# Kernel optimization log

Measured on AMD Instinct MI355X. Metric: run time of the kernel, lower is better.

Reference implementation:

```python
import jax, jax.numpy as jnp
import numpy as np

NUM_GRID = 16
GRID_SIZE = 8  # 128 / NUM_GRID
H = W = 128
BN_EPS = 1e-5


def conv2d(x, w, b, pad):
    y = jax.lax.conv_general_dilated(
        x, w, window_strides=(1, 1), padding=[(pad, pad), (pad, pad)],
        dimension_numbers=('NCHW', 'OIHW', 'NCHW'))
    return y + b[None, :, None, None]


def bn(x, g, be, m, v):
    # inference-mode BatchNorm2d with running stats
    inv = g / jnp.sqrt(v + BN_EPS)
    return x * inv[None, :, None, None] + (be - m * inv)[None, :, None, None]


def setup_inputs() -> dict:
    key = jax.random.key(0)
    ks = jax.random.split(key, 6)
    def wconv(k, o, i, s):
        return jax.random.normal(k, (o, i, s, s), jnp.float32) * (1.0 / np.sqrt(i * s * s))
    return {
        'x': jax.random.uniform(ks[0], (64, 1, 128, 128), jnp.float32),
        'w1': wconv(ks[1], 64, 1, 3), 'b1': jnp.zeros((64,), jnp.float32),
        'g1': jnp.ones((64,), jnp.float32), 'be1': jnp.zeros((64,), jnp.float32),
        'm1': jnp.zeros((64,), jnp.float32), 'v1': jnp.ones((64,), jnp.float32),
        'w2': wconv(ks[2], 32, 64, 3), 'b2': jnp.zeros((32,), jnp.float32),
        'g2': jnp.ones((32,), jnp.float32), 'be2': jnp.zeros((32,), jnp.float32),
        'm2': jnp.zeros((32,), jnp.float32), 'v2': jnp.ones((32,), jnp.float32),
        'w3': wconv(ks[3], 32, 32, 3), 'b3': jnp.zeros((32,), jnp.float32),
        'g3': jnp.ones((32,), jnp.float32), 'be3': jnp.zeros((32,), jnp.float32),
        'm3': jnp.zeros((32,), jnp.float32), 'v3': jnp.ones((32,), jnp.float32),
        'w4': wconv(ks[4], 1, 32, 3), 'b4': jnp.zeros((1,), jnp.float32),
    }


def reference(x, w1, b1, g1, be1, m1, v1, w2, b2, g2, be2, m2, v2,
              w3, b3, g3, be3, m3, v3, w4, b4):
    # EncoderAttentionNodes.forward, phase='train', expressed with static shapes:
    # instead of torch.nonzero gather of valid grids, compute per-grid node
    # coordinates for ALL 16x16 grids and return a validity mask. The math per
    # valid grid is identical (the rect mask is a rectangular 8x8 block, so
    # masking + normalization reduce to block-local weighted sums).
    B = x.shape[0]
    h = jax.nn.relu(bn(conv2d(x, w1, b1, 4), g1, be1, m1, v1))   # [B,64,134,134]
    h = jax.nn.relu(bn(conv2d(h, w2, b2, 0), g2, be2, m2, v2))   # [B,32,132,132]
    h = jax.nn.relu(bn(conv2d(h, w3, b3, 0), g3, be3, m3, v3))   # [B,32,130,130]
    heat_raw = conv2d(h, w4, b4, 0)                              # [B,1,128,128]
    heat = jax.nn.sigmoid(heat_raw)[:, 0]                        # [B,128,128]

    # block view: [B, yi, ya, xj, xc] with yi,xj grid indices and ya,xc in-block
    hb = heat.reshape(B, NUM_GRID, GRID_SIZE, NUM_GRID, GRID_SIZE)
    grid = hb.max(axis=(2, 4)).reshape(B, NUM_GRID * NUM_GRID)   # maxpool 8x8 s8
    sorted_grid = jnp.sort(grid, axis=1)[:, ::-1]                # descending
    thresh = jnp.maximum(sorted_grid[:, 16], 0.9)[:, None]       # train phase
    valid = grid > thresh                                        # [B,256]

    xref = jnp.linspace(0.0, 1.0, W).reshape(NUM_GRID, GRID_SIZE)
    yref = jnp.linspace(0.0, 1.0, H).reshape(NUM_GRID, GRID_SIZE)
    s = hb.sum(axis=(2, 4))                                      # [B,16,16] block mass
    sx = jnp.einsum('biajc,jc->bij', hb, xref)
    sy = jnp.einsum('biajc,ia->bij', hb, yref)
    nodes = jnp.stack([sx / s, sy / s], axis=-1)                 # [B,16,16,2]
    nodes = nodes.reshape(B, NUM_GRID * NUM_GRID, 2)
    nodes = jnp.where(valid[:, :, None], nodes, 0.0)             # zero padded slots
    nodes_per_image = valid.sum(axis=1).astype(jnp.int32)        # == torch.bincount
    return nodes, heat_raw, valid, nodes_per_image
```

## Files before the change

kernel.cpp:

```cpp
#include <hip/hip_runtime.h>
#include <math.h>

#define BN_EPS 1e-5f

typedef _Float16 half8 __attribute__((ext_vector_type(8)));
typedef float f32x4 __attribute__((ext_vector_type(4)));

__global__ __launch_bounds__(256) void prep_kernel(
    const float* __restrict__ w1, const float* __restrict__ b1,
    const float* __restrict__ g1, const float* __restrict__ be1,
    const float* __restrict__ m1, const float* __restrict__ v1,
    const float* __restrict__ w2, const float* __restrict__ b2,
    const float* __restrict__ g2, const float* __restrict__ be2,
    const float* __restrict__ m2, const float* __restrict__ v2,
    const float* __restrict__ w3, const float* __restrict__ b3,
    const float* __restrict__ g3, const float* __restrict__ be3,
    const float* __restrict__ m3, const float* __restrict__ v3,
    char* __restrict__ ws)
{
    float* w1e = (float*)ws;
    float* b1e = (float*)(ws + 2304);
    float* b2e = (float*)(ws + 2560);
    float* b3e = (float*)(ws + 2688);
    _Float16* wT2e = (_Float16*)(ws + 2816);
    _Float16* wT3e = (_Float16*)(ws + 39680);

    for (int t = threadIdx.x; t < 576; t += 256) {
        int oc = t / 9;
        float inv = g1[oc] * rsqrtf(v1[oc] + BN_EPS);
        w1e[t] = w1[t] * inv;
    }
    for (int t = threadIdx.x; t < 64; t += 256) {
        float inv = g1[t] * rsqrtf(v1[t] + BN_EPS);
        b1e[t] = b1[t] * inv + be1[t] - m1[t] * inv;
    }
    for (int t = threadIdx.x; t < 32; t += 256) {
        float inv2 = g2[t] * rsqrtf(v2[t] + BN_EPS);
        b2e[t] = b2[t] * inv2 + be2[t] - m2[t] * inv2;
        float inv3 = g3[t] * rsqrtf(v3[t] + BN_EPS);
        b3e[t] = b3[t] * inv3 + be3[t] - m3[t] * inv3;
    }
    for (int t = threadIdx.x; t < 18432; t += 256) {
        int r = t / 2048; int rem = t - r * 2048;
        int oc = rem >> 6; int ic = rem & 63;
        float inv = g2[oc] * rsqrtf(v2[oc] + BN_EPS);
        wT2e[t] = (_Float16)(w2[(oc * 64 + ic) * 9 + r] * inv);
    }
    for (int t = threadIdx.x; t < 9216; t += 256) {
        int r = t / 1024; int rem = t - r * 1024;
        int oc = rem >> 5; int ic = rem & 31;
        float inv = g3[oc] * rsqrtf(v3[oc] + BN_EPS);
        wT3e[t] = (_Float16)(w3[(oc * 32 + ic) * 9 + r] * inv);
    }
}

__global__ __launch_bounds__(256, 3) void f12_kernel(
    const float* __restrict__ x, const char* __restrict__ wsw,
    _Float16* __restrict__ h2)
{
    const float* w1e = (const float*)wsw;
    const float* b1e = (const float*)(wsw + 2304);
    const float* b2e = (const float*)(wsw + 2560);
    const _Float16* wT2e = (const _Float16*)(wsw + 2816);

    constexpr int PSTR = 36;
    __shared__ float sX[20 * 20];
    __shared__ _Float16 sH1[324 * PSTR];

    const int t = threadIdx.x, lane = t & 63, w = t >> 6;
    const int tl = lane & 15, g = lane >> 4;
    const int img = blockIdx.z;
    const int x0 = blockIdx.x * 16, y0 = blockIdx.y * 16;

    const float* xb = x + (size_t)img * 16384;
    for (int idx = t; idx < 400; idx += 256) {
        int r = idx / 20, c = idx - r * 20;
        int iy = y0 - 4 + r, ix = x0 - 4 + c;
        sX[idx] = (iy >= 0 && iy < 128 && ix >= 0 && ix < 128)
                      ? xb[iy * 128 + ix] : 0.f;
    }
    __syncthreads();

    f32x4 acc[4][2];
#pragma unroll
    for (int pf = 0; pf < 4; pf++)
#pragma unroll
        for (int of = 0; of < 2; of++) acc[pf][of] = (f32x4){0.f, 0.f, 0.f, 0.f};

#pragma unroll
    for (int h = 0; h < 2; h++) {
        {
            const int ocg = __builtin_amdgcn_readfirstlane(t >> 6);
            const int pxslot = t & 63;
            float wreg[8][9];
            float bb[8];
#pragma unroll
            for (int j = 0; j < 8; j++) {
                int oc = h * 32 + ocg * 8 + j;
                bb[j] = b1e[oc];
#pragma unroll
                for (int k = 0; k < 9; k++) wreg[j][k] = w1e[oc * 9 + k];
            }
#pragma unroll
            for (int round = 0; round < 6; round++) {
                int px = pxslot + round * 64;
                if (px < 324) {
                    int py = px / 18, pxx = px - py * 18;
                    float a[9];
#pragma unroll
                    for (int ky = 0; ky < 3; ky++)
#pragma unroll
                        for (int kx = 0; kx < 3; kx++)
                            a[ky * 3 + kx] = sX[(py + ky) * 20 + pxx + kx];
                    half8 hv;
#pragma unroll
                    for (int j = 0; j < 8; j++) {
                        float acc1 = bb[j];
#pragma unroll
                        for (int k = 0; k < 9; k++)
                            acc1 = fmaf(a[k], wreg[j][k], acc1);
                        hv[j] = (_Float16)fmaxf(acc1, 0.f);
                    }
                    *(half8*)(&sH1[px * PSTR + ocg * 8]) = hv;
                }
            }
        }
        __syncthreads();

#pragma unroll
        for (int r = 0; r < 9; r++) {
            const int ky = r / 3, kx = r - ky * 3;
            half8 wf0 = *(const half8*)(
                wT2e + (r * 32 + tl) * 64 + h * 32 + g * 8);
            half8 wf1 = *(const half8*)(
                wT2e + (r * 32 + 16 + tl) * 64 + h * 32 + g * 8);
#pragma unroll
            for (int pf = 0; pf < 4; pf++) {
                const int yl = w * 4 + pf + ky;
                half8 af = *(const half8*)(
                    &sH1[(yl * 18 + tl + kx) * PSTR + g * 8]);
                acc[pf][0] = __builtin_amdgcn_mfma_f32_16x16x32_f16(
                    af, wf0, acc[pf][0], 0, 0, 0);
                acc[pf][1] = __builtin_amdgcn_mfma_f32_16x16x32_f16(
                    af, wf1, acc[pf][1], 0, 0, 0);
            }
        }
        if (h == 0) __syncthreads();
    }

    const float bb0 = b2e[tl], bb1 = b2e[16 + tl];
    _Float16* outb = h2 + (size_t)img * 132 * 132 * 32;
#pragma unroll
    for (int pf = 0; pf < 4; pf++) {
        int y = y0 + w * 4 + pf;
        if (y >= 132) continue;
#pragma unroll
        for (int i = 0; i < 4; i++) {
            int xc = x0 + 4 * g + i;
            if (xc >= 132) continue;
            _Float16* q = outb + ((size_t)y * 132 + xc) * 32 + tl;
            q[0]  = (_Float16)fmaxf(acc[pf][0][i] + bb0, 0.f);
            q[16] = (_Float16)fmaxf(acc[pf][1][i] + bb1, 0.f);
        }
    }
}

__global__ __launch_bounds__(256, 3) void conv3_kernel(
    const _Float16* __restrict__ in, const char* __restrict__ wsw,
    _Float16* __restrict__ out)
{
    const float* b3e = (const float*)(wsw + 2688);
    const _Float16* wT3e = (const _Float16*)(wsw + 39680);

    constexpr int HIN = 132, WIN = 132, HOUT = 130, WOUT = 130;
    constexpr int PSTR = 40;
    __shared__ _Float16 sIn[324 * PSTR];

    const int t = threadIdx.x, lane = t & 63, w = t >> 6;
    const int tl = lane & 15, g = lane >> 4;
    const int img = 63 - blockIdx.z;
    const int x0 = blockIdx.x * 16, y0 = blockIdx.y * 16;

    const _Float16* inb = in + (size_t)img * HIN * WIN * 32;

    for (int kk = 0; kk < 6; kk++) {
        int idx = t + kk * 256;
        if (idx < 1296) {
            int px = idx >> 2, sg = idx & 3;
            int py = px / 18, pxx = px - py * 18;
            int iy = y0 + py, ix = x0 + pxx;
            half8 v = (half8){0, 0, 0, 0, 0, 0, 0, 0};
            if (iy < HIN && ix < WIN)
                v = *(const half8*)(inb + ((size_t)iy * WIN + ix) * 32 + sg * 8);
            *(half8*)(&sIn[px * PSTR + sg * 8]) = v;
        }
    }

    f32x4 acc[4][2];
#pragma unroll
    for (int pf = 0; pf < 4; pf++)
#pragma unroll
        for (int of = 0; of < 2; of++) acc[pf][of] = (f32x4){0.f, 0.f, 0.f, 0.f};

    __syncthreads();

#pragma unroll
    for (int r = 0; r < 9; r++) {
        const int ky = r / 3, kx = r - ky * 3;
        half8 wf0 = *(const half8*)(wT3e + (r * 32 + tl) * 32 + g * 8);
        half8 wf1 = *(const half8*)(wT3e + (r * 32 + 16 + tl) * 32 + g * 8);
#pragma unroll
        for (int pf = 0; pf < 4; pf++) {
            const int yl = w * 4 + pf + ky;
            half8 af = *(const half8*)(&sIn[(yl * 18 + tl + kx) * PSTR + g * 8]);
            acc[pf][0] = __builtin_amdgcn_mfma_f32_16x16x32_f16(
                af, wf0, acc[pf][0], 0, 0, 0);
            acc[pf][1] = __builtin_amdgcn_mfma_f32_16x16x32_f16(
                af, wf1, acc[pf][1], 0, 0, 0);
        }
    }

    const float bb0 = b3e[tl], bb1 = b3e[16 + tl];
    _Float16* outb = out + (size_t)img * HOUT * WOUT * 32;
#pragma unroll
    for (int pf = 0; pf < 4; pf++) {
        int y = y0 + w * 4 + pf;
        if (y >= HOUT) continue;
#pragma unroll
        for (int i = 0; i < 4; i++) {
            int xc = x0 + 4 * g + i;
            if (xc >= WOUT) continue;
            _Float16* q = outb + ((size_t)y * WOUT + xc) * 32 + tl;
            q[0]  = (_Float16)fmaxf(acc[pf][0][i] + bb0, 0.f);
            q[16] = (_Float16)fmaxf(acc[pf][1][i] + bb1, 0.f);
        }
    }
}

__global__ __launch_bounds__(256) void conv4_kernel(
    const _Float16* __restrict__ h3, const float* __restrict__ w4,
    const float* __restrict__ b4, float* __restrict__ heat,
    float* __restrict__ stats)
{
    const int img = blockIdx.z;
    const int x0 = blockIdx.x * 16, y0 = blockIdx.y * 16;
    const int t = threadIdx.x;
    const int ty = t >> 4, tx = t & 15;

    __shared__ float sw[288];
    __shared__ float sS[256];
    for (int i = t; i < 288; i += 256) sw[i] = w4[i];
    __syncthreads();

    const int y = y0 + ty, x = x0 + tx;
    const _Float16* hb = h3 + (size_t)img * 130 * 130 * 32;
    float acc = b4[0];
#pragma unroll
    for (int r = 0; r < 9; r++) {
        const int ky = r / 3, kx = r - ky * 3;
        const _Float16* p = hb + ((size_t)(y + ky) * 130 + (x + kx)) * 32;
        half8 v0 = *(const half8*)(p);
        half8 v1 = *(const half8*)(p + 8);
        half8 v2 = *(const half8*)(p + 16);
        half8 v3 = *(const half8*)(p + 24);
#pragma unroll
        for (int j = 0; j < 8; j++) {
            acc = fmaf((float)v0[j], sw[(j) * 9 + r], acc);
            acc = fmaf((float)v1[j], sw[(8 + j) * 9 + r], acc);
            acc = fmaf((float)v2[j], sw[(16 + j) * 9 + r], acc);
            acc = fmaf((float)v3[j], sw[(24 + j) * 9 + r], acc);
        }
    }
    heat[(size_t)img * 16384 + y * 128 + x] = acc;
    sS[t] = 1.0f / (1.0f + expf(-acc));
    __syncthreads();

    const int w = t >> 6, l = t & 63;
    const int cy = w >> 1, cx = w & 1;
    const int ly = cy * 8 + (l >> 3), lx = cx * 8 + (l & 7);
    float v = sS[ly * 16 + lx];
    float mx = v, s = v;
    float sx = v * ((float)(x0 + lx) * (1.0f / 127.0f));
    float sy = v * ((float)(y0 + ly) * (1.0f / 127.0f));
#pragma unroll
    for (int off = 1; off < 64; off <<= 1) {
        mx = fmaxf(mx, __shfl_xor(mx, off));
        s += __shfl_xor(s, off);
        sx += __shfl_xor(sx, off);
        sy += __shfl_xor(sy, off);
    }
    if (l == 0) {
        int cell = (blockIdx.y * 2 + cy) * 16 + blockIdx.x * 2 + cx;
        float4* st = (float4*)(stats + ((size_t)img * 256 + cell) * 4);
        *st = make_float4(mx, s, sx, sy);
    }
}

__global__ __launch_bounds__(256) void nodes2_kernel(
    const float* __restrict__ stats, float* __restrict__ nodes,
    float* __restrict__ valid, float* __restrict__ counts)
{
    int b = blockIdx.x;
    int gsl = threadIdx.x;
    float4 st = ((const float4*)stats)[b * 256 + gsl];
    float mx = st.x, s = st.y, sx = st.z, sy = st.w;

    __shared__ float gv[256];
    gv[gsl] = mx;
    __syncthreads();

    int cgt = 0, ceq = 0;
    for (int j = 0; j < 256; j++) {
        float vj = gv[j];
        cgt += (vj > mx) ? 1 : 0;
        ceq += (vj == mx) ? 1 : 0;
    }
    __shared__ float kth;
    if (cgt <= 16 && 16 < cgt + ceq) kth = mx;
    __syncthreads();

    float thresh = fmaxf(kth, 0.9f);
    bool val = mx > thresh;
    nodes[((size_t)b * 256 + gsl) * 2 + 0] = val ? sx / s : 0.f;
    nodes[((size_t)b * 256 + gsl) * 2 + 1] = val ? sy / s : 0.f;
    valid[(size_t)b * 256 + gsl] = val ? 1.f : 0.f;

    unsigned long long ball = __ballot(val);
    __shared__ int wc[4];
    if ((gsl & 63) == 0) wc[gsl >> 6] = __popcll(ball);
    __syncthreads();
    if (gsl == 0) counts[b] = (float)(wc[0] + wc[1] + wc[2] + wc[3]);
}

extern "C" void kernel_launch(void* const* d_in, const int* in_sizes, int n_in,
                              void* d_out, int out_size, void* d_ws, size_t ws_size,
                              hipStream_t stream)
{
    const float* x   = (const float*)d_in[0];
    const float* w1  = (const float*)d_in[1];
    const float* b1  = (const float*)d_in[2];
    const float* g1  = (const float*)d_in[3];
    const float* be1 = (const float*)d_in[4];
    const float* m1  = (const float*)d_in[5];
    const float* v1  = (const float*)d_in[6];
    const float* w2  = (const float*)d_in[7];
    const float* b2  = (const float*)d_in[8];
    const float* g2  = (const float*)d_in[9];
    const float* be2 = (const float*)d_in[10];
    const float* m2  = (const float*)d_in[11];
    const float* v2  = (const float*)d_in[12];
    const float* w3  = (const float*)d_in[13];
    const float* b3  = (const float*)d_in[14];
    const float* g3  = (const float*)d_in[15];
    const float* be3 = (const float*)d_in[16];
    const float* m3  = (const float*)d_in[17];
    const float* v3  = (const float*)d_in[18];
    const float* w4  = (const float*)d_in[19];
    const float* b4  = (const float*)d_in[20];

    float* out = (float*)d_out;
    float* out_nodes = out;
    float* out_heat  = out + 32768;
    float* out_valid = out + 32768 + 1048576;
    float* out_count = out + 32768 + 1048576 + 16384;

    char* ws = (char*)d_ws;
    const size_t WREGION = 65536;
    float* stats = (float*)(ws + WREGION);
    _Float16* h2 = (_Float16*)(ws + WREGION + 262144);
    _Float16* h3 = h2 + (size_t)64 * 17424 * 32;

    prep_kernel<<<1, 256, 0, stream>>>(w1, b1, g1, be1, m1, v1,
                                       w2, b2, g2, be2, m2, v2,
                                       w3, b3, g3, be3, m3, v3, ws);

    dim3 gd(9, 9, 64);
    f12_kernel<<<gd, 256, 0, stream>>>(x, ws, h2);
    conv3_kernel<<<gd, 256, 0, stream>>>(h2, ws, h3);

    dim3 gd4(8, 8, 64);
    conv4_kernel<<<gd4, 256, 0, stream>>>(h3, w4, b4, out_heat, stats);

    nodes2_kernel<<<64, 256, 0, stream>>>(stats, out_nodes, out_valid, out_count);
}
```

Baseline: 241.3 us.

## Use fp16 dot2 for conv1 and overlap second conv1 half with conv2 MFMA

Conv1 weights are prepacked as fp16 pairs and the input tile is held in fp16 LDS, so each output channel needs five fdot2 instructions instead of nine fp32 FMAs. The second half of conv1 is computed into registers while the MFMA pass for the first half runs, and is written to shared memory only after a barrier. This hides scalar conv1 work behind matrix work. In exchange it holds more registers (occupancy hint drops from 3 to 2 blocks) and lowers conv1 input and weight precision to fp16.

```diff
diff --git a/kernel.cpp b/kernel.cpp
--- a/kernel.cpp
+++ b/kernel.cpp
@@ -4,7 +4,19 @@
 #define BN_EPS 1e-5f
 
 typedef _Float16 half8 __attribute__((ext_vector_type(8)));
+typedef _Float16 half2v __attribute__((ext_vector_type(2)));
 typedef float f32x4 __attribute__((ext_vector_type(4)));
+
+#if __has_builtin(__builtin_amdgcn_fdot2)
+#define FDOT2(a, b, c) __builtin_amdgcn_fdot2((a), (b), (c), false)
+#else
+#define FDOT2(a, b, c) \
+    fmaf((float)(a)[0], (float)(b)[0], fmaf((float)(a)[1], (float)(b)[1], (c)))
+#endif
+
+static __device__ inline half2v u2h(unsigned int u) {
+    union { unsigned int x; half2v h; } c; c.x = u; return c.h;
+}
 
 __global__ __launch_bounds__(256) void prep_kernel(
     const float* __restrict__ w1, const float* __restrict__ b1,
@@ -18,21 +30,27 @@
     const float* __restrict__ m3, const float* __restrict__ v3,
     char* __restrict__ ws)
 {
-    float* w1e = (float*)ws;
     float* b1e = (float*)(ws + 2304);
     float* b2e = (float*)(ws + 2560);
     float* b3e = (float*)(ws + 2688);
     _Float16* wT2e = (_Float16*)(ws + 2816);
     _Float16* wT3e = (_Float16*)(ws + 39680);
-
-    for (int t = threadIdx.x; t < 576; t += 256) {
-        int oc = t / 9;
-        float inv = g1[oc] * rsqrtf(v1[oc] + BN_EPS);
-        w1e[t] = w1[t] * inv;
-    }
+    unsigned int* w1p = (unsigned int*)(ws + 58112);
+
     for (int t = threadIdx.x; t < 64; t += 256) {
         float inv = g1[t] * rsqrtf(v1[t] + BN_EPS);
         b1e[t] = b1[t] * inv + be1[t] - m1[t] * inv;
+    }
+    for (int t = threadIdx.x; t < 320; t += 256) {
+        int oc = t / 5, p = t - oc * 5;
+        float inv = g1[oc] * rsqrtf(v1[oc] + BN_EPS);
+        int k0 = 2 * p, k1 = 2 * p + 1;
+        _Float16 h0 = (k0 < 9) ? (_Float16)(w1[oc * 9 + k0] * inv) : (_Float16)0.f;
+        _Float16 h1 = (k1 < 9) ? (_Float16)(w1[oc * 9 + k1] * inv) : (_Float16)0.f;
+        unsigned short u0, u1;
+        __builtin_memcpy(&u0, &h0, 2);
+        __builtin_memcpy(&u1, &h1, 2);
+        w1p[t] = (unsigned int)u0 | ((unsigned int)u1 << 16);
     }
     for (int t = threadIdx.x; t < 32; t += 256) {
         float inv2 = g2[t] * rsqrtf(v2[t] + BN_EPS);
@@ -54,17 +72,17 @@
     }
 }
 
-__global__ __launch_bounds__(256, 3) void f12_kernel(
+__global__ __launch_bounds__(256, 2) void f12_kernel(
     const float* __restrict__ x, const char* __restrict__ wsw,
     _Float16* __restrict__ h2)
 {
-    const float* w1e = (const float*)wsw;
     const float* b1e = (const float*)(wsw + 2304);
     const float* b2e = (const float*)(wsw + 2560);
     const _Float16* wT2e = (const _Float16*)(wsw + 2816);
+    const unsigned int* w1p = (const unsigned int*)(wsw + 58112);
 
     constexpr int PSTR = 36;
-    __shared__ float sX[20 * 20];
+    __shared__ _Float16 sXh[400];
     __shared__ _Float16 sH1[324 * PSTR];
 
     const int t = threadIdx.x, lane = t & 63, w = t >> 6;
@@ -76,10 +94,14 @@
     for (int idx = t; idx < 400; idx += 256) {
         int r = idx / 20, c = idx - r * 20;
         int iy = y0 - 4 + r, ix = x0 - 4 + c;
-        sX[idx] = (iy >= 0 && iy < 128 && ix >= 0 && ix < 128)
+        float v = (iy >= 0 && iy < 128 && ix >= 0 && ix < 128)
                       ? xb[iy * 128 + ix] : 0.f;
-    }
-    __syncthreads();
+        sXh[idx] = (_Float16)v;
+    }
+    __syncthreads();
+
+    const int ocg = __builtin_amdgcn_readfirstlane(t >> 6);
+    const int slot = t & 63;
 
     f32x4 acc[4][2];
 #pragma unroll
@@ -87,46 +109,59 @@
 #pragma unroll
         for (int of = 0; of < 2; of++) acc[pf][of] = (f32x4){0.f, 0.f, 0.f, 0.f};
 
-#pragma unroll
-    for (int h = 0; h < 2; h++) {
-        {
-            const int ocg = __builtin_amdgcn_readfirstlane(t >> 6);
-            const int pxslot = t & 63;
-            float wreg[8][9];
-            float bb[8];
+    half8 rr[6];
+
+    auto c1_compute = [&](int h) {
+        unsigned int wp[8][5];
+        float bb[8];
+#pragma unroll
+        for (int j = 0; j < 8; j++) {
+            int oc = h * 32 + ocg * 8 + j;
+            bb[j] = b1e[oc];
+#pragma unroll
+            for (int p = 0; p < 5; p++) wp[j][p] = w1p[oc * 5 + p];
+        }
+#pragma unroll
+        for (int round = 0; round < 6; round++) {
+            int px = slot + round * 64;
+            int pc = (px < 324) ? px : 0;
+            int py = pc / 18, pxx = pc - py * 18;
+            _Float16 tv[9];
+#pragma unroll
+            for (int r3 = 0; r3 < 3; r3++)
+#pragma unroll
+                for (int c3 = 0; c3 < 3; c3++)
+                    tv[r3 * 3 + c3] = sXh[(py + r3) * 20 + pxx + c3];
+            half2v a0 = {tv[0], tv[1]};
+            half2v a1 = {tv[2], tv[3]};
+            half2v a2 = {tv[4], tv[5]};
+            half2v a3 = {tv[6], tv[7]};
+            half2v a4 = {tv[8], (_Float16)0.f};
+            half8 q;
 #pragma unroll
             for (int j = 0; j < 8; j++) {
-                int oc = h * 32 + ocg * 8 + j;
-                bb[j] = b1e[oc];
-#pragma unroll
-                for (int k = 0; k < 9; k++) wreg[j][k] = w1e[oc * 9 + k];
+                float f = bb[j];
+                f = FDOT2(a0, u2h(wp[j][0]), f);
+                f = FDOT2(a1, u2h(wp[j][1]), f);
+                f = FDOT2(a2, u2h(wp[j][2]), f);
+                f = FDOT2(a3, u2h(wp[j][3]), f);
+                f = FDOT2(a4, u2h(wp[j][4]), f);
+                q[j] = (_Float16)fmaxf(f, 0.f);
             }
-#pragma unroll
-            for (int round = 0; round < 6; round++) {
-                int px = pxslot + round * 64;
-                if (px < 324) {
-                    int py = px / 18, pxx = px - py * 18;
-                    float a[9];
-#pragma unroll
-                    for (int ky = 0; ky < 3; ky++)
-#pragma unroll
-                        for (int kx = 0; kx < 3; kx++)
-                            a[ky * 3 + kx] = sX[(py + ky) * 20 + pxx + kx];
-                    half8 hv;
-#pragma unroll
-                    for (int j = 0; j < 8; j++) {
-                        float acc1 = bb[j];
-#pragma unroll
-                        for (int k = 0; k < 9; k++)
-                            acc1 = fmaf(a[k], wreg[j][k], acc1);
-                        hv[j] = (_Float16)fmaxf(acc1, 0.f);
-                    }
-                    *(half8*)(&sH1[px * PSTR + ocg * 8]) = hv;
-                }
-            }
-        }
-        __syncthreads();
-
+            rr[round] = q;
+        }
+    };
+
+    auto c1_store = [&]() {
+#pragma unroll
+        for (int round = 0; round < 6; round++) {
+            int px = slot + round * 64;
+            if (px < 324)
+                *(half8*)(&sH1[px * PSTR + ocg * 8]) = rr[round];
+        }
+    };
+
+    auto c2_mfma = [&](int h) {
 #pragma unroll
         for (int r = 0; r < 9; r++) {
             const int ky = r / 3, kx = r - ky * 3;
@@ -145,8 +180,19 @@
                     af, wf1, acc[pf][1], 0, 0, 0);
             }
         }
-        if (h == 0) __syncthreads();
-    }
+    };
+
+    c1_compute(0);
+    c1_store();
+    __syncthreads();
+
+    c1_compute(1);
+    c2_mfma(0);
+    __syncthreads();
+
+    c1_store();
+    __syncthreads();
+    c2_mfma(1);
 
     const float bb0 = b2e[tl], bb1 = b2e[16 + tl];
     _Float16* outb = h2 + (size_t)img * 132 * 132 * 32;
```

After: 260.5 us. 8.0% more time.

## Fuse conv3 and conv4 into one kernel, keeping h3 tile in shared memory

Applied to the files above, without the earlier changes.

Merges the conv3 and conv4 kernels so each block computes an 18x18 halo tile of conv3 output directly from global h2 and stores it in LDS, then runs conv4 and the per-cell statistics from LDS. This removes the global round trip for the h3 intermediate and one kernel launch. In exchange, halo pixels are recomputed (324 vs 256 per tile), conv3 inputs are read straight from global/cache rather than staged in LDS, and occupancy drops to 2 blocks per CU.

```diff
diff --git a/kernel.cpp b/kernel.cpp
--- a/kernel.cpp
+++ b/kernel.cpp
@@ -165,100 +165,67 @@
     }
 }
 
-__global__ __launch_bounds__(256, 3) void conv3_kernel(
-    const _Float16* __restrict__ in, const char* __restrict__ wsw,
-    _Float16* __restrict__ out)
+__global__ __launch_bounds__(256, 2) void f34_kernel(
+    const _Float16* __restrict__ h2, const char* __restrict__ wsw,
+    const float* __restrict__ w4, const float* __restrict__ b4,
+    float* __restrict__ heat, float* __restrict__ stats)
 {
     const float* b3e = (const float*)(wsw + 2688);
     const _Float16* wT3e = (const _Float16*)(wsw + 39680);
 
-    constexpr int HIN = 132, WIN = 132, HOUT = 130, WOUT = 130;
-    constexpr int PSTR = 40;
-    __shared__ _Float16 sIn[324 * PSTR];
+    constexpr int PSTR = 36;
+    __shared__ _Float16 sH3[324 * PSTR];
+    __shared__ float sw[288];
+    __shared__ float sS[256];
 
     const int t = threadIdx.x, lane = t & 63, w = t >> 6;
     const int tl = lane & 15, g = lane >> 4;
     const int img = 63 - blockIdx.z;
     const int x0 = blockIdx.x * 16, y0 = blockIdx.y * 16;
 
-    const _Float16* inb = in + (size_t)img * HIN * WIN * 32;
-
-    for (int kk = 0; kk < 6; kk++) {
-        int idx = t + kk * 256;
-        if (idx < 1296) {
-            int px = idx >> 2, sg = idx & 3;
-            int py = px / 18, pxx = px - py * 18;
-            int iy = y0 + py, ix = x0 + pxx;
-            half8 v = (half8){0, 0, 0, 0, 0, 0, 0, 0};
-            if (iy < HIN && ix < WIN)
-                v = *(const half8*)(inb + ((size_t)iy * WIN + ix) * 32 + sg * 8);
-            *(half8*)(&sIn[px * PSTR + sg * 8]) = v;
-        }
-    }
-
-    f32x4 acc[4][2];
-#pragma unroll
-    for (int pf = 0; pf < 4; pf++)
-#pragma unroll
-        for (int of = 0; of < 2; of++) acc[pf][of] = (f32x4){0.f, 0.f, 0.f, 0.f};
-
-    __syncthreads();
-
+    for (int i = t; i < 288; i += 256) sw[i] = w4[i];
+
+    const _Float16* inb = h2 + (size_t)img * 132 * 132 * 32;
+    const float bb0 = b3e[tl], bb1 = b3e[16 + tl];
+
+#pragma unroll
+    for (int tt = 0; tt < 6; tt++) {
+        const int m = w + 4 * tt;
+        if (m < 21) {
+            int px = m * 16 + tl;
+            if (px > 323) px = 323;
+            const int py = px / 18, pxx = px - py * 18;
+            const _Float16* base =
+                inb + ((size_t)(y0 + py) * 132 + (x0 + pxx)) * 32 + g * 8;
+            f32x4 c0 = (f32x4){0.f, 0.f, 0.f, 0.f};
+            f32x4 c1 = (f32x4){0.f, 0.f, 0.f, 0.f};
+#pragma unroll
+            for (int r = 0; r < 9; r++) {
+                const int ky = r / 3, kx = r - ky * 3;
+                half8 wf0 = *(const half8*)(wT3e + (r * 32 + tl) * 32 + g * 8);
+                half8 wf1 = *(const half8*)(wT3e + (r * 32 + 16 + tl) * 32 + g * 8);
+                half8 af = *(const half8*)(base + ((size_t)ky * 132 + kx) * 32);
+                c0 = __builtin_amdgcn_mfma_f32_16x16x32_f16(af, wf0, c0, 0, 0, 0);
+                c1 = __builtin_amdgcn_mfma_f32_16x16x32_f16(af, wf1, c1, 0, 0, 0);
+            }
+#pragma unroll
+            for (int i = 0; i < 4; i++) {
+                const int px_d = m * 16 + 4 * g + i;
+                if (px_d < 324) {
+                    sH3[px_d * PSTR + tl] = (_Float16)fmaxf(c0[i] + bb0, 0.f);
+                    sH3[px_d * PSTR + 16 + tl] = (_Float16)fmaxf(c1[i] + bb1, 0.f);
+                }
+            }
+        }
+    }
+    __syncthreads();
+
+    const int ty = t >> 4, tx = t & 15;
+    float acc = b4[0];
 #pragma unroll
     for (int r = 0; r < 9; r++) {
         const int ky = r / 3, kx = r - ky * 3;
-        half8 wf0 = *(const half8*)(wT3e + (r * 32 + tl) * 32 + g * 8);
-        half8 wf1 = *(const half8*)(wT3e + (r * 32 + 16 + tl) * 32 + g * 8);
-#pragma unroll
-        for (int pf = 0; pf < 4; pf++) {
-            const int yl = w * 4 + pf + ky;
-            half8 af = *(const half8*)(&sIn[(yl * 18 + tl + kx) * PSTR + g * 8]);
-            acc[pf][0] = __builtin_amdgcn_mfma_f32_16x16x32_f16(
-                af, wf0, acc[pf][0], 0, 0, 0);
-            acc[pf][1] = __builtin_amdgcn_mfma_f32_16x16x32_f16(
-                af, wf1, acc[pf][1], 0, 0, 0);
-        }
-    }
-
-    const float bb0 = b3e[tl], bb1 = b3e[16 + tl];
-    _Float16* outb = out + (size_t)img * HOUT * WOUT * 32;
-#pragma unroll
-    for (int pf = 0; pf < 4; pf++) {
-        int y = y0 + w * 4 + pf;
-        if (y >= HOUT) continue;
-#pragma unroll
-        for (int i = 0; i < 4; i++) {
-            int xc = x0 + 4 * g + i;
-            if (xc >= WOUT) continue;
-            _Float16* q = outb + ((size_t)y * WOUT + xc) * 32 + tl;
-            q[0]  = (_Float16)fmaxf(acc[pf][0][i] + bb0, 0.f);
-            q[16] = (_Float16)fmaxf(acc[pf][1][i] + bb1, 0.f);
-        }
-    }
-}
-
-__global__ __launch_bounds__(256) void conv4_kernel(
-    const _Float16* __restrict__ h3, const float* __restrict__ w4,
-    const float* __restrict__ b4, float* __restrict__ heat,
-    float* __restrict__ stats)
-{
-    const int img = blockIdx.z;
-    const int x0 = blockIdx.x * 16, y0 = blockIdx.y * 16;
-    const int t = threadIdx.x;
-    const int ty = t >> 4, tx = t & 15;
-
-    __shared__ float sw[288];
-    __shared__ float sS[256];
-    for (int i = t; i < 288; i += 256) sw[i] = w4[i];
-    __syncthreads();
-
-    const int y = y0 + ty, x = x0 + tx;
-    const _Float16* hb = h3 + (size_t)img * 130 * 130 * 32;
-    float acc = b4[0];
-#pragma unroll
-    for (int r = 0; r < 9; r++) {
-        const int ky = r / 3, kx = r - ky * 3;
-        const _Float16* p = hb + ((size_t)(y + ky) * 130 + (x + kx)) * 32;
+        const _Float16* p = &sH3[((ty + ky) * 18 + tx + kx) * PSTR];
         half8 v0 = *(const half8*)(p);
         half8 v1 = *(const half8*)(p + 8);
         half8 v2 = *(const half8*)(p + 16);
@@ -271,12 +238,12 @@
             acc = fmaf((float)v3[j], sw[(24 + j) * 9 + r], acc);
         }
     }
-    heat[(size_t)img * 16384 + y * 128 + x] = acc;
+    heat[(size_t)img * 16384 + (y0 + ty) * 128 + (x0 + tx)] = acc;
     sS[t] = 1.0f / (1.0f + expf(-acc));
     __syncthreads();
 
-    const int w = t >> 6, l = t & 63;
-    const int cy = w >> 1, cx = w & 1;
+    const int wv = t >> 6, l = t & 63;
+    const int cy = wv >> 1, cx = wv & 1;
     const int ly = cy * 8 + (l >> 3), lx = cx * 8 + (l & 7);
     float v = sS[ly * 16 + lx];
     float mx = v, s = v;
@@ -368,7 +335,6 @@
     const size_t WREGION = 65536;
     float* stats = (float*)(ws + WREGION);
     _Float16* h2 = (_Float16*)(ws + WREGION + 262144);
-    _Float16* h3 = h2 + (size_t)64 * 17424 * 32;
 
     prep_kernel<<<1, 256, 0, stream>>>(w1, b1, g1, be1, m1, v1,
                                        w2, b2, g2, be2, m2, v2,
@@ -376,10 +342,9 @@
 
     dim3 gd(9, 9, 64);
     f12_kernel<<<gd, 256, 0, stream>>>(x, ws, h2);
-    conv3_kernel<<<gd, 256, 0, stream>>>(h2, ws, h3);
-
-    dim3 gd4(8, 8, 64);
-    conv4_kernel<<<gd4, 256, 0, stream>>>(h3, w4, b4, out_heat, stats);
+
+    dim3 gd34(8, 8, 64);
+    f34_kernel<<<gd34, 256, 0, stream>>>(h2, ws, w4, b4, out_heat, stats);
 
     nodes2_kernel<<<64, 256, 0, stream>>>(stats, out_nodes, out_valid, out_count);
 }
```

Result: slower. 322.8 us (+33.7%).

## Warp-specialize f12 kernel into producer/consumer pipeline over three x-tiles

Applied to the files above, without the earlier changes.

Restructures the fused conv1+conv2 kernel into 512-thread blocks. Four producer waves compute conv1 activations into a double-buffered shared tile, while four consumer waves run the MFMA conv2 on the previous buffer. The consumer waves also prefetch the next input tile and write outputs. Each block now walks three horizontal tiles in six stages, aiming to overlap scalar conv1 work with the matrix-core conv2. The cost is twice the shared memory, fewer blocks in flight, and an extra pipeline fill and drain stage per block.

```diff
diff --git a/kernel.cpp b/kernel.cpp
--- a/kernel.cpp
+++ b/kernel.cpp
@@ -54,7 +54,7 @@
     }
 }
 
-__global__ __launch_bounds__(256, 3) void f12_kernel(
+__global__ __launch_bounds__(512, 2) void f12_kernel(
     const float* __restrict__ x, const char* __restrict__ wsw,
     _Float16* __restrict__ h2)
 {
@@ -64,20 +64,33 @@
     const _Float16* wT2e = (const _Float16*)(wsw + 2816);
 
     constexpr int PSTR = 36;
-    __shared__ float sX[20 * 20];
-    __shared__ _Float16 sH1[324 * PSTR];
-
-    const int t = threadIdx.x, lane = t & 63, w = t >> 6;
+    constexpr int TX = 3, NS = 2 * TX;
+    __shared__ float sX[2][400];
+    __shared__ _Float16 sH1[2][324 * PSTR];
+
+    const int t = threadIdx.x;
+    const bool isP = t < 256;
+    const int img = blockIdx.z;
+    const int bx = blockIdx.x, ty = blockIdx.y;
+    const int y0 = ty * 16;
+
+    const float* xb = x + (size_t)img * 16384;
+
+    const int t2 = t & 255;
+    const int cw = t2 >> 6;
+    const int lane = t2 & 63;
     const int tl = lane & 15, g = lane >> 4;
-    const int img = blockIdx.z;
-    const int x0 = blockIdx.x * 16, y0 = blockIdx.y * 16;
-
-    const float* xb = x + (size_t)img * 16384;
-    for (int idx = t; idx < 400; idx += 256) {
-        int r = idx / 20, c = idx - r * 20;
-        int iy = y0 - 4 + r, ix = x0 - 4 + c;
-        sX[idx] = (iy >= 0 && iy < 128 && ix >= 0 && ix < 128)
-                      ? xb[iy * 128 + ix] : 0.f;
+    const int ocg = __builtin_amdgcn_readfirstlane(t2 >> 6);
+    const int pxslot = t2 & 63;
+
+    {
+        const int x0 = bx * TX * 16;
+        for (int idx = t; idx < 400; idx += 512) {
+            int r = idx / 20, c = idx - r * 20;
+            int iy = y0 - 4 + r, ix = x0 - 4 + c;
+            sX[0][idx] = (iy >= 0 && iy < 128 && ix >= 0 && ix < 128)
+                             ? xb[iy * 128 + ix] : 0.f;
+        }
     }
     __syncthreads();
 
@@ -87,81 +100,110 @@
 #pragma unroll
         for (int of = 0; of < 2; of++) acc[pf][of] = (f32x4){0.f, 0.f, 0.f, 0.f};
 
-#pragma unroll
-    for (int h = 0; h < 2; h++) {
-        {
-            const int ocg = __builtin_amdgcn_readfirstlane(t >> 6);
-            const int pxslot = t & 63;
-            float wreg[8][9];
-            float bb[8];
-#pragma unroll
-            for (int j = 0; j < 8; j++) {
-                int oc = h * 32 + ocg * 8 + j;
-                bb[j] = b1e[oc];
-#pragma unroll
-                for (int k = 0; k < 9; k++) wreg[j][k] = w1e[oc * 9 + k];
-            }
-#pragma unroll
-            for (int round = 0; round < 6; round++) {
-                int px = pxslot + round * 64;
-                if (px < 324) {
-                    int py = px / 18, pxx = px - py * 18;
-                    float a[9];
-#pragma unroll
-                    for (int ky = 0; ky < 3; ky++)
-#pragma unroll
-                        for (int kx = 0; kx < 3; kx++)
-                            a[ky * 3 + kx] = sX[(py + ky) * 20 + pxx + kx];
-                    half8 hv;
-#pragma unroll
-                    for (int j = 0; j < 8; j++) {
-                        float acc1 = bb[j];
-#pragma unroll
-                        for (int k = 0; k < 9; k++)
-                            acc1 = fmaf(a[k], wreg[j][k], acc1);
-                        hv[j] = (_Float16)fmaxf(acc1, 0.f);
+    const float bb0 = b2e[tl], bb1 = b2e[16 + tl];
+    _Float16* outb = h2 + (size_t)img * 132 * 132 * 32;
+
+    for (int p = 0; p <= NS; ++p) {
+        if (isP) {
+            if (p < NS) {
+                const int tile = p >> 1, h = p & 1;
+                const float* sxb = sX[tile & 1];
+                _Float16* dst = sH1[p & 1];
+                float wreg[8][9];
+                float bbp[8];
+#pragma unroll
+                for (int j = 0; j < 8; j++) {
+                    int oc = h * 32 + ocg * 8 + j;
+                    bbp[j] = b1e[oc];
+#pragma unroll
+                    for (int k = 0; k < 9; k++) wreg[j][k] = w1e[oc * 9 + k];
+                }
+#pragma unroll
+                for (int round = 0; round < 6; round++) {
+                    int px = pxslot + round * 64;
+                    if (px < 324) {
+                        int py = px / 18, pxx = px - py * 18;
+                        float a[9];
+#pragma unroll
+                        for (int ky = 0; ky < 3; ky++)
+#pragma unroll
+                            for (int kx = 0; kx < 3; kx++)
+                                a[ky * 3 + kx] = sxb[(py + ky) * 20 + pxx + kx];
+                        half8 hv;
+#pragma unroll
+                        for (int j = 0; j < 8; j++) {
+                            float acc1 = bbp[j];
+#pragma unroll
+                            for (int k = 0; k < 9; k++)
+                                acc1 = fmaf(a[k], wreg[j][k], acc1);
+                            hv[j] = (_Float16)fmaxf(acc1, 0.f);
+                        }
+                        *(half8*)(&dst[px * PSTR + ocg * 8]) = hv;
                     }
-                    *(half8*)(&sH1[px * PSTR + ocg * 8]) = hv;
                 }
             }
-        }
-        __syncthreads();
-
-#pragma unroll
-        for (int r = 0; r < 9; r++) {
-            const int ky = r / 3, kx = r - ky * 3;
-            half8 wf0 = *(const half8*)(
-                wT2e + (r * 32 + tl) * 64 + h * 32 + g * 8);
-            half8 wf1 = *(const half8*)(
-                wT2e + (r * 32 + 16 + tl) * 64 + h * 32 + g * 8);
-#pragma unroll
-            for (int pf = 0; pf < 4; pf++) {
-                const int yl = w * 4 + pf + ky;
-                half8 af = *(const half8*)(
-                    &sH1[(yl * 18 + tl + kx) * PSTR + g * 8]);
-                acc[pf][0] = __builtin_amdgcn_mfma_f32_16x16x32_f16(
-                    af, wf0, acc[pf][0], 0, 0, 0);
-                acc[pf][1] = __builtin_amdgcn_mfma_f32_16x16x32_f16(
-                    af, wf1, acc[pf][1], 0, 0, 0);
+        } else {
+            if (p >= 1) {
+                const int s = p - 1;
+                const int tile = s >> 1, h = s & 1;
+                const _Float16* src = sH1[s & 1];
+#pragma unroll
+                for (int r = 0; r < 9; r++) {
+                    const int ky = r / 3, kx = r - ky * 3;
+                    half8 wf0 = *(const half8*)(
+                        wT2e + (r * 32 + tl) * 64 + h * 32 + g * 8);
+                    half8 wf1 = *(const half8*)(
+                        wT2e + (r * 32 + 16 + tl) * 64 + h * 32 + g * 8);
+#pragma unroll
+                    for (int pf = 0; pf < 4; pf++) {
+                        const int yl = cw * 4 + pf + ky;
+                        half8 af = *(const half8*)(
+                            &src[(yl * 18 + tl + kx) * PSTR + g * 8]);
+                        acc[pf][0] = __builtin_amdgcn_mfma_f32_16x16x32_f16(
+                            af, wf0, acc[pf][0], 0, 0, 0);
+                        acc[pf][1] = __builtin_amdgcn_mfma_f32_16x16x32_f16(
+                            af, wf1, acc[pf][1], 0, 0, 0);
+                    }
+                }
+                if (h == 1) {
+                    const int x0 = (bx * TX + tile) * 16;
+#pragma unroll
+                    for (int pf = 0; pf < 4; pf++) {
+                        int y = y0 + cw * 4 + pf;
+                        if (y < 132) {
+#pragma unroll
+                            for (int i = 0; i < 4; i++) {
+                                int xc = x0 + 4 * g + i;
+                                if (xc < 132) {
+                                    _Float16* q =
+                                        outb + ((size_t)y * 132 + xc) * 32 + tl;
+                                    q[0] = (_Float16)fmaxf(
+                                        acc[pf][0][i] + bb0, 0.f);
+                                    q[16] = (_Float16)fmaxf(
+                                        acc[pf][1][i] + bb1, 0.f);
+                                }
+                            }
+                        }
+                        acc[pf][0] = (f32x4){0.f, 0.f, 0.f, 0.f};
+                        acc[pf][1] = (f32x4){0.f, 0.f, 0.f, 0.f};
+                    }
+                } else {
+                    const int tile_next = tile + 1;
+                    if (tile_next < TX) {
+                        const int x0n = (bx * TX + tile_next) * 16;
+                        float* dstx = sX[tile_next & 1];
+                        for (int idx = t2; idx < 400; idx += 256) {
+                            int r = idx / 20, c = idx - r * 20;
+                            int iy = y0 - 4 + r, ix = x0n - 4 + c;
+                            dstx[idx] =
+                                (iy >= 0 && iy < 128 && ix >= 0 && ix < 128)
+                                    ? xb[iy * 128 + ix] : 0.f;
+                        }
+                    }
+                }
             }
         }
-        if (h == 0) __syncthreads();
-    }
-
-    const float bb0 = b2e[tl], bb1 = b2e[16 + tl];
-    _Float16* outb = h2 + (size_t)img * 132 * 132 * 32;
-#pragma unroll
-    for (int pf = 0; pf < 4; pf++) {
-        int y = y0 + w * 4 + pf;
-        if (y >= 132) continue;
-#pragma unroll
-        for (int i = 0; i < 4; i++) {
-            int xc = x0 + 4 * g + i;
-            if (xc >= 132) continue;
-            _Float16* q = outb + ((size_t)y * 132 + xc) * 32 + tl;
-            q[0]  = (_Float16)fmaxf(acc[pf][0][i] + bb0, 0.f);
-            q[16] = (_Float16)fmaxf(acc[pf][1][i] + bb1, 0.f);
-        }
+        if (p < NS) __syncthreads();
     }
 }
 
@@ -374,8 +416,10 @@
                                        w2, b2, g2, be2, m2, v2,
                                        w3, b3, g3, be3, m3, v3, ws);
 
+    dim3 gdf(3, 9, 64);
+    f12_kernel<<<gdf, 512, 0, stream>>>(x, ws, h2);
+
     dim3 gd(9, 9, 64);
-    f12_kernel<<<gd, 256, 0, stream>>>(x, ws, h2);
     conv3_kernel<<<gd, 256, 0, stream>>>(h2, ws, h3);
 
     dim3 gd4(8, 8, 64);
```

Result: slower. 326.9 us (+35.5%).
